# Performance work log

Hardware: AMD Instinct MI355X
Metric: run time of the kernel (lower is better)

Reference implementation:

```python
import jax, jax.numpy as jnp
import numpy as np

SCENARIO_DIM = 10
ACTION_DIM = 2
N_EXPERTS = 8
EXP_H = 32
GATE_H = 64
B = 1048576


def setup_inputs() -> dict:
    key = jax.random.key(0)
    ks = jax.random.split(key, 16)
    s = 0.1
    return {
        "x": jax.random.normal(ks[0], (B, SCENARIO_DIM), dtype=jnp.float32),
        # stacked expert MLP params: Linear(10->32), Linear(32->32), Linear(32->2)
        "W1": jax.random.normal(ks[1], (N_EXPERTS, SCENARIO_DIM, EXP_H), dtype=jnp.float32) * s,
        "b1": jax.random.normal(ks[2], (N_EXPERTS, EXP_H), dtype=jnp.float32) * s,
        "W2": jax.random.normal(ks[3], (N_EXPERTS, EXP_H, EXP_H), dtype=jnp.float32) * s,
        "b2": jax.random.normal(ks[4], (N_EXPERTS, EXP_H), dtype=jnp.float32) * s,
        "W3": jax.random.normal(ks[5], (N_EXPERTS, EXP_H, ACTION_DIM), dtype=jnp.float32) * s,
        "b3": jax.random.normal(ks[6], (N_EXPERTS, ACTION_DIM), dtype=jnp.float32) * s,
        # gating: Linear(10->64), Linear(64->n_experts)
        "G1": jax.random.normal(ks[7], (SCENARIO_DIM, GATE_H), dtype=jnp.float32) * s,
        "gb1": jax.random.normal(ks[8], (GATE_H,), dtype=jnp.float32) * s,
        "G2": jax.random.normal(ks[9], (GATE_H, N_EXPERTS), dtype=jnp.float32) * s,
        "gb2": jax.random.normal(ks[10], (N_EXPERTS,), dtype=jnp.float32) * s,
        # refine: Linear(2+10->64), Linear(64->2)
        "R1": jax.random.normal(ks[11], (ACTION_DIM + SCENARIO_DIM, GATE_H), dtype=jnp.float32) * s,
        "rb1": jax.random.normal(ks[12], (GATE_H,), dtype=jnp.float32) * s,
        "R2": jax.random.normal(ks[13], (GATE_H, ACTION_DIM), dtype=jnp.float32) * s,
        "rb2": jax.random.normal(ks[14], (ACTION_DIM,), dtype=jnp.float32) * s,
    }


def reference(x, W1, b1, W2, b2, W3, b3, G1, gb1, G2, gb2, R1, rb1, R2, rb2):
    # batched expert MLPs: (B, E, H)
    h = jax.nn.relu(jnp.einsum("bd,edh->beh", x, W1) + b1)
    h = jax.nn.relu(jnp.einsum("beh,ehk->bek", h, W2) + b2)
    outs = jnp.tanh(jnp.einsum("beh,eha->bea", h, W3) + b3)  # (B, E, A)
    # gating softmax over experts
    g = jax.nn.relu(x @ G1 + gb1)
    w = jax.nn.softmax(g @ G2 + gb2, axis=-1)  # (B, E)
    fused = jnp.einsum("bea,be->ba", outs, w)  # (B, A)
    # refine head
    r = jax.nn.relu(jnp.concatenate([fused, x], axis=-1) @ R1 + rb1)
    return jnp.tanh(r @ R2 + rb2)
```

## Files before the change

### kernel.cpp

```cpp
#include <hip/hip_runtime.h>


#define B_TOTAL 1048576
#define NFRAG   60
#define FRAG_U4 (NFRAG * 64)

typedef _Float16 f16x8 __attribute__((ext_vector_type(8)));
typedef __fp16   fp16x2 __attribute__((ext_vector_type(2)));
typedef float    f32x16 __attribute__((ext_vector_type(16)));
typedef unsigned int u32x4v __attribute__((ext_vector_type(4)));

#define MFMA(a, b, c) __builtin_amdgcn_mfma_f32_32x32x16_f16((a), (b), (c), 0, 0, 0)

__device__ __forceinline__ unsigned pkrtz(float a, float b) {
    fp16x2 h = __builtin_amdgcn_cvt_pkrtz(a, b);
    return __builtin_bit_cast(unsigned, h);
}
__device__ __forceinline__ f16x8 mk4(unsigned a, unsigned b, unsigned c, unsigned d) {
    u32x4v t; t.x = a; t.y = b; t.z = c; t.w = d;
    return __builtin_bit_cast(f16x8, t);
}
__device__ __forceinline__ f32x16 zero16() {
    f32x16 z;
    #pragma unroll
    for (int i = 0; i < 16; ++i) z[i] = 0.f;
    return z;
}
__device__ __forceinline__ void packrelu(const f32x16& c, unsigned* p) {
    #pragma unroll
    for (int i = 0; i < 8; ++i)
        p[i] = pkrtz(fmaxf(c[2 * i], 0.f), fmaxf(c[2 * i + 1], 0.f));
}
__device__ __forceinline__ float tanh_fast(float v) {
    v = fminf(fmaxf(v, -10.f), 10.f);
    float e = __expf(2.f * v);
    return __fdividef(e - 1.f, e + 1.f);
}

__global__ void prep_kernel(const float* __restrict__ W1, const float* __restrict__ b1,
                            const float* __restrict__ W2, const float* __restrict__ b2,
                            const float* __restrict__ W3, const float* __restrict__ b3,
                            const float* __restrict__ G1, const float* __restrict__ gb1,
                            const float* __restrict__ G2, const float* __restrict__ gb2,
                            const float* __restrict__ R1, const float* __restrict__ rb1,
                            const float* __restrict__ R2, const float* __restrict__ rb2,
                            _Float16* __restrict__ ws)
{
    int gid = blockIdx.x * 256 + threadIdx.x;
    if (gid >= NFRAG * 64) return;
    int f = gid >> 6, lane = gid & 63;
    int m = lane & 31, h = lane >> 5;
    float v[8];
    #pragma unroll
    for (int j = 0; j < 8; ++j) v[j] = 0.f;

    if (f < 2) {
        int mo = f * 32 + m;
        for (int j = 0; j < 8; ++j) {
            if (h == 0)       v[j] = G1[j * 64 + mo];
            else if (j < 2)   v[j] = G1[(8 + j) * 64 + mo];
            else if (j == 2)  v[j] = gb1[mo];
        }
    } else if (f < 6) {
        int s = f - 2;
        for (int j = 0; j < 8; ++j) {
            int k = 32 * (s >> 1) + 16 * (s & 1) + (j & 3) + 8 * (j >> 2) + 4 * h;
            v[j] = (m < 8) ? G2[k * 8 + m] : 0.f;
        }
    } else if (f < 8) {
        int mo = (f - 6) * 32 + m;
        for (int j = 0; j < 8; ++j) {
            if (h == 0)       v[j] = R1[j * 64 + mo];
            else if (j < 4)   v[j] = R1[(8 + j) * 64 + mo];
            else if (j == 4)  v[j] = rb1[mo];
        }
    } else if (f < 12) {
        int s = f - 8;
        for (int j = 0; j < 8; ++j) {
            int k = 32 * (s >> 1) + 16 * (s & 1) + (j & 3) + 8 * (j >> 2) + 4 * h;
            v[j] = (m < 2) ? R2[k * 2 + m] : 0.f;
        }
    } else {
        int e = (f - 12) / 6, t = (f - 12) % 6;
        if (t == 0) {
            for (int j = 0; j < 8; ++j) {
                if (h == 0)       v[j] = W1[e * 320 + j * 32 + m];
                else if (j < 2)   v[j] = W1[e * 320 + (8 + j) * 32 + m];
                else if (j == 2)  v[j] = b1[e * 32 + m];
            }
        } else if (t == 1 || t == 2) {
            int s = t - 1;
            for (int j = 0; j < 8; ++j) {
                int k = 16 * s + (j & 3) + 8 * (j >> 2) + 4 * h;
                v[j] = W2[e * 1024 + k * 32 + m];
            }
        } else if (t == 3) {
            if (h == 0) v[0] = b2[e * 32 + m];
        } else {
            int s = t - 4;
            for (int j = 0; j < 8; ++j) {
                int k = 16 * s + (j & 3) + 8 * (j >> 2) + 4 * h;
                v[j] = (m < 2) ? W3[e * 64 + k * 2 + m] : 0.f;
            }
        }
    }
    _Float16* dst = ws + (size_t)(f * 64 + lane) * 8;
    #pragma unroll
    for (int j = 0; j < 8; ++j) dst[j] = (_Float16)v[j];
}

__global__ __launch_bounds__(1024) void brain_mfma(
    const float* __restrict__ x,
    const u32x4v* __restrict__ wsf,
    const float* __restrict__ b3, const float* __restrict__ gb2,
    const float* __restrict__ rb2,
    float* __restrict__ out)
{
    __shared__ u32x4v smem[FRAG_U4];
    const int tid = threadIdx.x;
    for (int i = tid; i < FRAG_U4; i += 1024) smem[i] = wsf[i];
    __syncthreads();

    const int lane = tid & 63;
    const int wv   = tid >> 6;
    const int n    = lane & 31;
    const int h    = lane >> 5;
    const size_t sample = (size_t)blockIdx.x * 512 + wv * 32 + n;

    const float2* xp = (const float2*)(x + sample * 10);
    float2 a0 = xp[h ? 3 : 0];
    float2 a1 = xp[h ? 4 : 1];
    float2 a2 = xp[h ? 4 : 2];
    float2 a3 = xp[3];

    const unsigned ONEZERO = 0x00003C00u;
    unsigned pk_a = pkrtz(a0.x, a0.y);
    unsigned pk_b = pkrtz(a1.x, a1.y);
    unsigned pk_c = pkrtz(a2.x, a2.y);
    unsigned pk_d = pkrtz(a3.x, a3.y);

    f16x8 xfrag = h ? mk4(pk_b, ONEZERO, 0u, 0u) : mk4(pk_a, pk_b, pk_c, pk_d);
    unsigned rx1 = h ? pk_b : pk_a;
    unsigned rx2 = h ? ONEZERO : pk_b;
    unsigned rx3 = h ? 0u : pk_c;
    unsigned rx0_hi = pk_a;

    const f16x8 ONES = mk4(0x3C003C00u, 0x3C003C00u, 0x3C003C00u, 0x3C003C00u);
    #define FRAG(F) __builtin_bit_cast(f16x8, smem[(F) * 64 + lane])

    float w[8];
    {
        f32x16 cg0 = MFMA(FRAG(0), xfrag, zero16());
        f32x16 cg1 = MFMA(FRAG(1), xfrag, zero16());
        unsigned p0[8], p1[8];
        packrelu(cg0, p0);
        packrelu(cg1, p1);
        f32x16 cl = MFMA(FRAG(2), mk4(p0[0], p0[1], p0[2], p0[3]), zero16());
        cl = MFMA(FRAG(3), mk4(p0[4], p0[5], p0[6], p0[7]), cl);
        cl = MFMA(FRAG(4), mk4(p1[0], p1[1], p1[2], p1[3]), cl);
        cl = MFMA(FRAG(5), mk4(p1[4], p1[5], p1[6], p1[7]), cl);
        float l[8];
        #pragma unroll
        for (int j = 0; j < 4; ++j) {
            l[j]     = cl[j] + gb2[j];
            l[4 + j] = __shfl_xor(cl[j], 32) + gb2[4 + j];
        }
        float mx = l[0];
        #pragma unroll
        for (int j = 1; j < 8; ++j) mx = fmaxf(mx, l[j]);
        float s = 0.f;
        #pragma unroll
        for (int j = 0; j < 8; ++j) { w[j] = __expf(l[j] - mx); s += w[j]; }
        float inv = __fdividef(1.f, s);
        #pragma unroll
        for (int j = 0; j < 8; ++j) w[j] *= inv;
    }

    float fused0 = 0.f, fused1 = 0.f;
    #pragma unroll 1
    for (int e = 0; e < 8; ++e) {
        const int fb = 12 + e * 6;
        f32x16 c1 = MFMA(FRAG(fb), xfrag, zero16());
        unsigned q[8];
        packrelu(c1, q);
        f32x16 c2 = MFMA(FRAG(fb + 1), mk4(q[0], q[1], q[2], q[3]), zero16());
        c2 = MFMA(FRAG(fb + 2), mk4(q[4], q[5], q[6], q[7]), c2);
        c2 = MFMA(FRAG(fb + 3), ONES, c2);
        packrelu(c2, q);
        f32x16 c3 = MFMA(FRAG(fb + 4), mk4(q[0], q[1], q[2], q[3]), zero16());
        c3 = MFMA(FRAG(fb + 5), mk4(q[4], q[5], q[6], q[7]), c3);
        float o0 = tanh_fast(c3[0] + b3[2 * e]);
        float o1 = tanh_fast(c3[1] + b3[2 * e + 1]);
        fused0 = fmaf(w[e], o0, fused0);
        fused1 = fmaf(w[e], o1, fused1);
    }

    unsigned rx0 = h ? rx0_hi : pkrtz(fused0, fused1);
    f16x8 rfrag = mk4(rx0, rx1, rx2, rx3);
    f32x16 cr0 = MFMA(FRAG(6), rfrag, zero16());
    f32x16 cr1 = MFMA(FRAG(7), rfrag, zero16());
    unsigned p0[8], p1[8];
    packrelu(cr0, p0);
    packrelu(cr1, p1);
    f32x16 cd = MFMA(FRAG(8), mk4(p0[0], p0[1], p0[2], p0[3]), zero16());
    cd = MFMA(FRAG(9),  mk4(p0[4], p0[5], p0[6], p0[7]), cd);
    cd = MFMA(FRAG(10), mk4(p1[0], p1[1], p1[2], p1[3]), cd);
    cd = MFMA(FRAG(11), mk4(p1[4], p1[5], p1[6], p1[7]), cd);

    if (h == 0) {
        float2 o;
        o.x = tanh_fast(cd[0] + rb2[0]);
        o.y = tanh_fast(cd[1] + rb2[1]);
        ((float2*)out)[sample] = o;
    }
}

extern "C" void kernel_launch(void* const* d_in, const int* in_sizes, int n_in,
                              void* d_out, int out_size, void* d_ws, size_t ws_size,
                              hipStream_t stream) {
    const float* x   = (const float*)d_in[0];
    const float* W1  = (const float*)d_in[1];
    const float* b1  = (const float*)d_in[2];
    const float* W2  = (const float*)d_in[3];
    const float* b2  = (const float*)d_in[4];
    const float* W3  = (const float*)d_in[5];
    const float* b3  = (const float*)d_in[6];
    const float* G1  = (const float*)d_in[7];
    const float* gb1 = (const float*)d_in[8];
    const float* G2  = (const float*)d_in[9];
    const float* gb2 = (const float*)d_in[10];
    const float* R1  = (const float*)d_in[11];
    const float* rb1 = (const float*)d_in[12];
    const float* R2  = (const float*)d_in[13];
    const float* rb2 = (const float*)d_in[14];
    float* out = (float*)d_out;
    _Float16* ws = (_Float16*)d_ws;

    hipLaunchKernelGGL(prep_kernel, dim3(15), dim3(256), 0, stream,
                       W1, b1, W2, b2, W3, b3, G1, gb1, G2, gb2, R1, rb1, R2, rb2, ws);
    hipLaunchKernelGGL(brain_mfma, dim3(B_TOTAL / 512), dim3(1024), 0, stream,
                       x, (const u32x4v*)ws, b3, gb2, rb2, out);
}
```

Baseline: 180.6 us.

## Process two 32-sample tiles per wave to reuse weight fragments and interleave MFMAs

Each wave now handles 64 samples as two independent 32-sample tiles, A and B. Each weight fragment read from LDS feeds two MFMAs, and the two tiles' chains interleave to hide MFMA latency. The grid is halved, so the per-block LDS weight fill is spread over twice as many samples. ReLU is now applied after packing to half precision with a packed f16 max, and launch bounds request 4 blocks of 1024 threads, which raises register pressure and risks spills.

```diff
diff --git a/kernel.cpp b/kernel.cpp
--- a/kernel.cpp
+++ b/kernel.cpp
@@ -12,24 +12,24 @@
 
 #define MFMA(a, b, c) __builtin_amdgcn_mfma_f32_32x32x16_f16((a), (b), (c), 0, 0, 0)
 
-__device__ __forceinline__ unsigned pkrtz(float a, float b) {
-    fp16x2 h = __builtin_amdgcn_cvt_pkrtz(a, b);
-    return __builtin_bit_cast(unsigned, h);
+__device__ __forceinline__ unsigned pkrtz_u(float a, float b) {
+    fp16x2 t = __builtin_amdgcn_cvt_pkrtz(a, b);
+    return __builtin_bit_cast(unsigned, t);
+}
+__device__ __forceinline__ unsigned pkru(float a, float b) {
+    fp16x2 t = __builtin_amdgcn_cvt_pkrtz(a, b);
+    fp16x2 z = {(__fp16)0.f, (__fp16)0.f};
+    fp16x2 m = __builtin_elementwise_max(t, z);
+    return __builtin_bit_cast(unsigned, m);
 }
 __device__ __forceinline__ f16x8 mk4(unsigned a, unsigned b, unsigned c, unsigned d) {
     u32x4v t; t.x = a; t.y = b; t.z = c; t.w = d;
     return __builtin_bit_cast(f16x8, t);
 }
-__device__ __forceinline__ f32x16 zero16() {
-    f32x16 z;
-    #pragma unroll
-    for (int i = 0; i < 16; ++i) z[i] = 0.f;
-    return z;
-}
 __device__ __forceinline__ void packrelu(const f32x16& c, unsigned* p) {
     #pragma unroll
     for (int i = 0; i < 8; ++i)
-        p[i] = pkrtz(fmaxf(c[2 * i], 0.f), fmaxf(c[2 * i + 1], 0.f));
+        p[i] = pkru(c[2 * i], c[2 * i + 1]);
 }
 __device__ __forceinline__ float tanh_fast(float v) {
     v = fminf(fmaxf(v, -10.f), 10.f);
@@ -109,7 +109,7 @@
     for (int j = 0; j < 8; ++j) dst[j] = (_Float16)v[j];
 }
 
-__global__ __launch_bounds__(1024) void brain_mfma(
+__global__ __launch_bounds__(1024, 4) void brain_mfma(
     const float* __restrict__ x,
     const u32x4v* __restrict__ wsf,
     const float* __restrict__ b3, const float* __restrict__ gb2,
@@ -125,93 +125,136 @@
     const int wv   = tid >> 6;
     const int n    = lane & 31;
     const int h    = lane >> 5;
-    const size_t sample = (size_t)blockIdx.x * 512 + wv * 32 + n;
-
-    const float2* xp = (const float2*)(x + sample * 10);
-    float2 a0 = xp[h ? 3 : 0];
-    float2 a1 = xp[h ? 4 : 1];
-    float2 a2 = xp[h ? 4 : 2];
-    float2 a3 = xp[3];
+    const size_t sA = (size_t)blockIdx.x * 1024 + wv * 64 + n;
+    const size_t sB = sA + 32;
 
     const unsigned ONEZERO = 0x00003C00u;
-    unsigned pk_a = pkrtz(a0.x, a0.y);
-    unsigned pk_b = pkrtz(a1.x, a1.y);
-    unsigned pk_c = pkrtz(a2.x, a2.y);
-    unsigned pk_d = pkrtz(a3.x, a3.y);
-
-    f16x8 xfrag = h ? mk4(pk_b, ONEZERO, 0u, 0u) : mk4(pk_a, pk_b, pk_c, pk_d);
-    unsigned rx1 = h ? pk_b : pk_a;
-    unsigned rx2 = h ? ONEZERO : pk_b;
-    unsigned rx3 = h ? 0u : pk_c;
-    unsigned rx0_hi = pk_a;
+
+    const float2* xpA = (const float2*)(x + sA * 10);
+    const float2* xpB = (const float2*)(x + sB * 10);
+    float2 A0 = xpA[h ? 3 : 0], A1 = xpA[h ? 4 : 1], A2 = xpA[h ? 4 : 2], A3 = xpA[3];
+    float2 B0 = xpB[h ? 3 : 0], B1 = xpB[h ? 4 : 1], B2 = xpB[h ? 4 : 2], B3 = xpB[3];
+
+    unsigned pkAa = pkrtz_u(A0.x, A0.y), pkAb = pkrtz_u(A1.x, A1.y);
+    unsigned pkAc = pkrtz_u(A2.x, A2.y), pkAd = pkrtz_u(A3.x, A3.y);
+    unsigned pkBa = pkrtz_u(B0.x, B0.y), pkBb = pkrtz_u(B1.x, B1.y);
+    unsigned pkBc = pkrtz_u(B2.x, B2.y), pkBd = pkrtz_u(B3.x, B3.y);
+
+    f16x8 xfA = h ? mk4(pkAb, ONEZERO, 0u, 0u) : mk4(pkAa, pkAb, pkAc, pkAd);
+    f16x8 xfB = h ? mk4(pkBb, ONEZERO, 0u, 0u) : mk4(pkBa, pkBb, pkBc, pkBd);
+    unsigned rxA1 = h ? pkAb : pkAa, rxA2 = h ? ONEZERO : pkAb, rxA3 = h ? 0u : pkAc;
+    unsigned rxB1 = h ? pkBb : pkBa, rxB2 = h ? ONEZERO : pkBb, rxB3 = h ? 0u : pkBc;
+    unsigned rxA0_hi = pkAa, rxB0_hi = pkBa;
 
     const f16x8 ONES = mk4(0x3C003C00u, 0x3C003C00u, 0x3C003C00u, 0x3C003C00u);
+    f32x16 Z;
+    #pragma unroll
+    for (int i = 0; i < 16; ++i) Z[i] = 0.f;
+
     #define FRAG(F) __builtin_bit_cast(f16x8, smem[(F) * 64 + lane])
 
-    float w[8];
+    float wA[8], wB[8];
     {
-        f32x16 cg0 = MFMA(FRAG(0), xfrag, zero16());
-        f32x16 cg1 = MFMA(FRAG(1), xfrag, zero16());
-        unsigned p0[8], p1[8];
-        packrelu(cg0, p0);
-        packrelu(cg1, p1);
-        f32x16 cl = MFMA(FRAG(2), mk4(p0[0], p0[1], p0[2], p0[3]), zero16());
-        cl = MFMA(FRAG(3), mk4(p0[4], p0[5], p0[6], p0[7]), cl);
-        cl = MFMA(FRAG(4), mk4(p1[0], p1[1], p1[2], p1[3]), cl);
-        cl = MFMA(FRAG(5), mk4(p1[4], p1[5], p1[6], p1[7]), cl);
-        float l[8];
-        #pragma unroll
-        for (int j = 0; j < 4; ++j) {
-            l[j]     = cl[j] + gb2[j];
-            l[4 + j] = __shfl_xor(cl[j], 32) + gb2[4 + j];
-        }
-        float mx = l[0];
-        #pragma unroll
-        for (int j = 1; j < 8; ++j) mx = fmaxf(mx, l[j]);
-        float s = 0.f;
-        #pragma unroll
-        for (int j = 0; j < 8; ++j) { w[j] = __expf(l[j] - mx); s += w[j]; }
-        float inv = __fdividef(1.f, s);
-        #pragma unroll
-        for (int j = 0; j < 8; ++j) w[j] *= inv;
-    }
-
-    float fused0 = 0.f, fused1 = 0.f;
+        f16x8 g0 = FRAG(0), g1 = FRAG(1);
+        f32x16 cg0A = MFMA(g0, xfA, Z), cg1A = MFMA(g1, xfA, Z);
+        f32x16 cg0B = MFMA(g0, xfB, Z), cg1B = MFMA(g1, xfB, Z);
+        unsigned p0A[8], p1A[8], p0B[8], p1B[8];
+        packrelu(cg0A, p0A); packrelu(cg1A, p1A);
+        packrelu(cg0B, p0B); packrelu(cg1B, p1B);
+        f16x8 l0 = FRAG(2), l1 = FRAG(3), l2 = FRAG(4), l3 = FRAG(5);
+        f32x16 clA = MFMA(l0, mk4(p0A[0], p0A[1], p0A[2], p0A[3]), Z);
+        clA = MFMA(l1, mk4(p0A[4], p0A[5], p0A[6], p0A[7]), clA);
+        clA = MFMA(l2, mk4(p1A[0], p1A[1], p1A[2], p1A[3]), clA);
+        clA = MFMA(l3, mk4(p1A[4], p1A[5], p1A[6], p1A[7]), clA);
+        f32x16 clB = MFMA(l0, mk4(p0B[0], p0B[1], p0B[2], p0B[3]), Z);
+        clB = MFMA(l1, mk4(p0B[4], p0B[5], p0B[6], p0B[7]), clB);
+        clB = MFMA(l2, mk4(p1B[0], p1B[1], p1B[2], p1B[3]), clB);
+        clB = MFMA(l3, mk4(p1B[4], p1B[5], p1B[6], p1B[7]), clB);
+
+        #pragma unroll 1
+        for (int t = 0; t < 2; ++t) {
+            const f32x16& cl = t ? clB : clA;
+            float* w = t ? wB : wA;
+            float l[8];
+            #pragma unroll
+            for (int j = 0; j < 4; ++j) {
+                l[j]     = cl[j] + gb2[j];
+                l[4 + j] = __shfl_xor(cl[j], 32) + gb2[4 + j];
+            }
+            float mx = l[0];
+            #pragma unroll
+            for (int j = 1; j < 8; ++j) mx = fmaxf(mx, l[j]);
+            float s = 0.f;
+            #pragma unroll
+            for (int j = 0; j < 8; ++j) { w[j] = __expf(l[j] - mx); s += w[j]; }
+            float inv = __fdividef(1.f, s);
+            #pragma unroll
+            for (int j = 0; j < 8; ++j) w[j] *= inv;
+        }
+    }
+
+    float fA0 = 0.f, fA1 = 0.f, fB0 = 0.f, fB1 = 0.f;
     #pragma unroll 1
     for (int e = 0; e < 8; ++e) {
         const int fb = 12 + e * 6;
-        f32x16 c1 = MFMA(FRAG(fb), xfrag, zero16());
-        unsigned q[8];
-        packrelu(c1, q);
-        f32x16 c2 = MFMA(FRAG(fb + 1), mk4(q[0], q[1], q[2], q[3]), zero16());
-        c2 = MFMA(FRAG(fb + 2), mk4(q[4], q[5], q[6], q[7]), c2);
-        c2 = MFMA(FRAG(fb + 3), ONES, c2);
-        packrelu(c2, q);
-        f32x16 c3 = MFMA(FRAG(fb + 4), mk4(q[0], q[1], q[2], q[3]), zero16());
-        c3 = MFMA(FRAG(fb + 5), mk4(q[4], q[5], q[6], q[7]), c3);
-        float o0 = tanh_fast(c3[0] + b3[2 * e]);
-        float o1 = tanh_fast(c3[1] + b3[2 * e + 1]);
-        fused0 = fmaf(w[e], o0, fused0);
-        fused1 = fmaf(w[e], o1, fused1);
-    }
-
-    unsigned rx0 = h ? rx0_hi : pkrtz(fused0, fused1);
-    f16x8 rfrag = mk4(rx0, rx1, rx2, rx3);
-    f32x16 cr0 = MFMA(FRAG(6), rfrag, zero16());
-    f32x16 cr1 = MFMA(FRAG(7), rfrag, zero16());
-    unsigned p0[8], p1[8];
-    packrelu(cr0, p0);
-    packrelu(cr1, p1);
-    f32x16 cd = MFMA(FRAG(8), mk4(p0[0], p0[1], p0[2], p0[3]), zero16());
-    cd = MFMA(FRAG(9),  mk4(p0[4], p0[5], p0[6], p0[7]), cd);
-    cd = MFMA(FRAG(10), mk4(p1[0], p1[1], p1[2], p1[3]), cd);
-    cd = MFMA(FRAG(11), mk4(p1[4], p1[5], p1[6], p1[7]), cd);
+        f16x8 a0 = FRAG(fb);
+        f32x16 c1A = MFMA(a0, xfA, Z);
+        f32x16 c1B = MFMA(a0, xfB, Z);
+        unsigned qA[8], qB[8];
+        packrelu(c1A, qA); packrelu(c1B, qB);
+
+        f16x8 a1 = FRAG(fb + 1), a2 = FRAG(fb + 2), a3 = FRAG(fb + 3);
+        f32x16 c2A = MFMA(a1, mk4(qA[0], qA[1], qA[2], qA[3]), Z);
+        c2A = MFMA(a2, mk4(qA[4], qA[5], qA[6], qA[7]), c2A);
+        c2A = MFMA(a3, ONES, c2A);
+        f32x16 c2B = MFMA(a1, mk4(qB[0], qB[1], qB[2], qB[3]), Z);
+        c2B = MFMA(a2, mk4(qB[4], qB[5], qB[6], qB[7]), c2B);
+        c2B = MFMA(a3, ONES, c2B);
+        packrelu(c2A, qA); packrelu(c2B, qB);
+
+        f16x8 a4 = FRAG(fb + 4), a5 = FRAG(fb + 5);
+        f32x16 c3A = MFMA(a4, mk4(qA[0], qA[1], qA[2], qA[3]), Z);
+        c3A = MFMA(a5, mk4(qA[4], qA[5], qA[6], qA[7]), c3A);
+        f32x16 c3B = MFMA(a4, mk4(qB[0], qB[1], qB[2], qB[3]), Z);
+        c3B = MFMA(a5, mk4(qB[4], qB[5], qB[6], qB[7]), c3B);
+
+        float b30 = b3[2 * e], b31 = b3[2 * e + 1];
+        fA0 = fmaf(wA[e], tanh_fast(c3A[0] + b30), fA0);
+        fA1 = fmaf(wA[e], tanh_fast(c3A[1] + b31), fA1);
+        fB0 = fmaf(wB[e], tanh_fast(c3B[0] + b30), fB0);
+        fB1 = fmaf(wB[e], tanh_fast(c3B[1] + b31), fB1);
+    }
+
+    unsigned rxA0 = h ? rxA0_hi : pkrtz_u(fA0, fA1);
+    unsigned rxB0 = h ? rxB0_hi : pkrtz_u(fB0, fB1);
+    f16x8 rfA = mk4(rxA0, rxA1, rxA2, rxA3);
+    f16x8 rfB = mk4(rxB0, rxB1, rxB2, rxB3);
+
+    f16x8 r0 = FRAG(6), r1 = FRAG(7);
+    f32x16 cr0A = MFMA(r0, rfA, Z), cr1A = MFMA(r1, rfA, Z);
+    f32x16 cr0B = MFMA(r0, rfB, Z), cr1B = MFMA(r1, rfB, Z);
+    unsigned p0A[8], p1A[8], p0B[8], p1B[8];
+    packrelu(cr0A, p0A); packrelu(cr1A, p1A);
+    packrelu(cr0B, p0B); packrelu(cr1B, p1B);
+
+    f16x8 d0 = FRAG(8), d1 = FRAG(9), d2 = FRAG(10), d3 = FRAG(11);
+    f32x16 cdA = MFMA(d0, mk4(p0A[0], p0A[1], p0A[2], p0A[3]), Z);
+    cdA = MFMA(d1, mk4(p0A[4], p0A[5], p0A[6], p0A[7]), cdA);
+    cdA = MFMA(d2, mk4(p1A[0], p1A[1], p1A[2], p1A[3]), cdA);
+    cdA = MFMA(d3, mk4(p1A[4], p1A[5], p1A[6], p1A[7]), cdA);
+    f32x16 cdB = MFMA(d0, mk4(p0B[0], p0B[1], p0B[2], p0B[3]), Z);
+    cdB = MFMA(d1, mk4(p0B[4], p0B[5], p0B[6], p0B[7]), cdB);
+    cdB = MFMA(d2, mk4(p1B[0], p1B[1], p1B[2], p1B[3]), cdB);
+    cdB = MFMA(d3, mk4(p1B[4], p1B[5], p1B[6], p1B[7]), cdB);
 
     if (h == 0) {
-        float2 o;
-        o.x = tanh_fast(cd[0] + rb2[0]);
-        o.y = tanh_fast(cd[1] + rb2[1]);
-        ((float2*)out)[sample] = o;
+        float2 oA, oB;
+        oA.x = tanh_fast(cdA[0] + rb2[0]);
+        oA.y = tanh_fast(cdA[1] + rb2[1]);
+        oB.x = tanh_fast(cdB[0] + rb2[0]);
+        oB.y = tanh_fast(cdB[1] + rb2[1]);
+        ((float2*)out)[sA] = oA;
+        ((float2*)out)[sB] = oB;
     }
 }
 
@@ -238,6 +281,6 @@
 
     hipLaunchKernelGGL(prep_kernel, dim3(15), dim3(256), 0, stream,
                        W1, b1, W2, b2, W3, b3, G1, gb1, G2, gb2, R1, rb1, R2, rb2, ws);
-    hipLaunchKernelGGL(brain_mfma, dim3(B_TOTAL / 512), dim3(1024), 0, stream,
+    hipLaunchKernelGGL(brain_mfma, dim3(B_TOTAL / 1024), dim3(1024), 0, stream,
                        x, (const u32x4v*)ws, b3, gb2, rb2, out);
 }
```

Result: faster. 168.9 us (-6.5%).
